# Optimization experiments

Hardware: AMD Instinct MI355X
Metric: run time of the kernel (lower is better)

The kernel has to match this reference:

```python
import math
import jax, jax.numpy as jnp
import numpy as np

B, T, D, L, E = 2, 1024, 1024, 12, 4
EPS = 1e-5


def _ln(v, g, b):
    mu = jnp.mean(v, axis=-1, keepdims=True)
    var = jnp.mean(jnp.square(v - mu), axis=-1, keepdims=True)
    return (v - mu) * jax.lax.rsqrt(var + EPS) * g + b


def setup_inputs() -> dict:
    key = jax.random.key(0)
    ks = jax.random.split(key, 4)
    x = jax.random.normal(ks[0], (B, T, D), dtype=jnp.float32)
    queries = jax.random.normal(ks[1], (L, D), dtype=jnp.float32) * 0.02
    W1 = jax.random.normal(ks[2], (L, D, E * D), dtype=jnp.float32) * 0.02
    W2 = jax.random.normal(ks[3], (L, E * D, D), dtype=jnp.float32) * 0.02
    return {
        'x': x,
        'queries': queries,
        'kn_g': jnp.ones((L, D), jnp.float32),
        'kn_b': jnp.zeros((L, D), jnp.float32),
        'ln_g': jnp.ones((L, D), jnp.float32),
        'ln_b': jnp.zeros((L, D), jnp.float32),
        'W1': W1,
        'b1': jnp.zeros((L, E * D), jnp.float32),
        'W2': W2,
        'b2': jnp.zeros((L, D), jnp.float32),
    }


def reference(x, queries, kn_g, kn_b, ln_g, ln_b, W1, b1, W2, b2):
    scale = 1.0 / math.sqrt(D)
    history = [x]
    h = x
    for l in range(L):
        V = jnp.stack(history, axis=0)              # (l+1, B, T, D)
        K = _ln(V, kn_g[l], kn_b[l])
        scores = jnp.einsum('d,lbtd->lbt', queries[l], K) * scale
        alpha = jax.nn.softmax(scores, axis=0)       # softmax over history axis
        residual = jnp.einsum('lbt,lbtd->btd', alpha, V)
        u = _ln(h, ln_g[l], ln_b[l])
        ff = jax.nn.gelu(u @ W1[l] + b1[l], approximate=False) @ W2[l] + b2[l]
        h = residual + ff
        history.append(h)
    return h
```

## Files before the change

kernel.cpp:

```cpp
#include <hip/hip_runtime.h>
#include <math.h>

#define BATCH 2
#define TSEQ 1024
#define DIM 1024
#define NLAYER 12
#define EDIM 4096
#define BT 2048
#define EPS_LN 1e-5f

typedef __attribute__((ext_vector_type(4))) float  f32x4;
typedef __attribute__((ext_vector_type(8))) __bf16 bf16x8;
typedef __attribute__((ext_vector_type(4))) __bf16 bf16x4;

__device__ __forceinline__ void gl_lds16(const void* gptr, void* lptr) {
    __builtin_amdgcn_global_load_lds(
        (const __attribute__((address_space(1))) void*)gptr,
        (__attribute__((address_space(3))) void*)lptr,
        16, 0, 0);
}

__global__ __launch_bounds__(256)
void attn_kernel(const float* __restrict__ x,
                 const float* __restrict__ hist,
                 const float* __restrict__ q,
                 const float* __restrict__ kng,
                 const float* __restrict__ knb,
                 const float* __restrict__ lng,
                 const float* __restrict__ lnb,
                 const float* __restrict__ b2,
                 float* __restrict__ hnext,
                 __bf16* __restrict__ u,
                 int nl)
{
    __shared__ float V[NLAYER][DIM];
    __shared__ float sS[NLAYER], sMu[NLAYER], sRs[NLAYER];

    const int bt = blockIdx.x;
    const int tid = threadIdx.x, lane = tid & 63, w = tid >> 6;

    f32x4 gqv[4];
    float sg = 0.f, sb = 0.f;
#pragma unroll
    for (int i = 0; i < 4; i++) {
        int d = i * 256 + lane * 4;
        f32x4 g4 = *(const f32x4*)(kng + d);
        f32x4 q4 = *(const f32x4*)(q + d);
        f32x4 b4 = *(const f32x4*)(knb + d);
#pragma unroll
        for (int c = 0; c < 4; c++) {
            float gq = g4[c] * q4[c];
            gqv[i][c] = gq;
            sg += gq;
            sb += b4[c] * q4[c];
        }
    }
#pragma unroll
    for (int off = 32; off; off >>= 1) {
        sg += __shfl_xor(sg, off);
        sb += __shfl_xor(sb, off);
    }

    for (int lp = w; lp < nl; lp += 4) {
        const float* vp = (lp == 0) ? (x + (size_t)bt * DIM)
                                    : (hist + ((size_t)lp * BT + bt) * DIM);
        f32x4 vv[4];
#pragma unroll
        for (int i = 0; i < 4; i++) vv[i] = *(const f32x4*)(vp + i * 256 + lane * 4);
        float s1 = 0.f, s2 = 0.f, sq = 0.f;
#pragma unroll
        for (int i = 0; i < 4; i++) {
            *(f32x4*)(&V[lp][i * 256 + lane * 4]) = vv[i];
#pragma unroll
            for (int c = 0; c < 4; c++) {
                float xv = vv[i][c];
                s1 += xv; s2 += xv * xv; sq += xv * gqv[i][c];
            }
        }
#pragma unroll
        for (int off = 32; off; off >>= 1) {
            s1 += __shfl_xor(s1, off);
            s2 += __shfl_xor(s2, off);
            sq += __shfl_xor(sq, off);
        }
        if (lane == 0) {
            float mu = s1 * (1.0f / DIM);
            float var = s2 * (1.0f / DIM) - mu * mu;
            float rs = rsqrtf(var + EPS_LN);
            sMu[lp] = mu; sRs[lp] = rs;
            sS[lp] = (rs * (sq - mu * sg) + sb) * (1.0f / 32.0f);
        }
    }
    __syncthreads();

    float mx = -1e30f;
#pragma unroll
    for (int i = 0; i < NLAYER; i++) if (i < nl) mx = fmaxf(mx, sS[i]);
    float al[NLAYER];
    float ssum = 0.f;
#pragma unroll
    for (int i = 0; i < NLAYER; i++) {
        al[i] = (i < nl) ? __expf(sS[i] - mx) : 0.f;
        ssum += al[i];
    }
    float inv = 1.0f / ssum;

    const int d = tid * 4;
    f32x4 r; r[0] = 0.f; r[1] = 0.f; r[2] = 0.f; r[3] = 0.f;
#pragma unroll
    for (int i = 0; i < NLAYER; i++) {
        if (i < nl) {
            f32x4 v4 = *(const f32x4*)(&V[i][d]);
            float a = al[i] * inv;
            r[0] += a * v4[0]; r[1] += a * v4[1]; r[2] += a * v4[2]; r[3] += a * v4[3];
        }
    }
    f32x4 h4 = *(const f32x4*)(&V[nl - 1][d]);
    f32x4 b24 = *(const f32x4*)(b2 + d);
    f32x4 ro; ro[0] = r[0] + b24[0]; ro[1] = r[1] + b24[1];
    ro[2] = r[2] + b24[2]; ro[3] = r[3] + b24[3];
    *(f32x4*)(hnext + (size_t)bt * DIM + d) = ro;

    float mu = sMu[nl - 1], rs = sRs[nl - 1];
    f32x4 g4 = *(const f32x4*)(lng + d);
    f32x4 b4 = *(const f32x4*)(lnb + d);
    bf16x4 uo;
#pragma unroll
    for (int c = 0; c < 4; c++) uo[c] = (__bf16)((h4[c] - mu) * rs * g4[c] + b4[c]);
    *(bf16x4*)(u + (size_t)bt * DIM + d) = uo;
}

__global__ __launch_bounds__(256) void wtrans_kernel(
    const float* __restrict__ W1, const float* __restrict__ W2,
    __bf16* __restrict__ W1t, __bf16* __restrict__ W2t)
{
    __shared__ float t[64][65];
    int z = blockIdx.z;
    const float* src; __bf16* dst; int R, C, rt, ct;
    if (z == 0) { src = W1; dst = W1t; R = DIM;  C = EDIM; rt = blockIdx.y; ct = blockIdx.x; }
    else        { src = W2; dst = W2t; R = EDIM; C = DIM;  rt = blockIdx.x; ct = blockIdx.y; }

    int tid = threadIdx.x;
    int lr = tid >> 2, cs = (tid & 3) << 4;
    const float* sp = src + (size_t)(rt * 64 + lr) * C + ct * 64 + cs;
#pragma unroll
    for (int s = 0; s < 4; s++) {
        f32x4 v = *(const f32x4*)(sp + s * 4);
        t[lr][cs + s * 4 + 0] = v[0];
        t[lr][cs + s * 4 + 1] = v[1];
        t[lr][cs + s * 4 + 2] = v[2];
        t[lr][cs + s * 4 + 3] = v[3];
    }
    __syncthreads();
    int oc = tid >> 2, rs = (tid & 3) << 4;
    bf16x8 o0, o1;
#pragma unroll
    for (int e = 0; e < 8; e++) o0[e] = (__bf16)t[rs + e][oc];
#pragma unroll
    for (int e = 0; e < 8; e++) o1[e] = (__bf16)t[rs + 8 + e][oc];
    __bf16* dp = dst + (size_t)(ct * 64 + oc) * R + rt * 64 + rs;
    *(bf16x8*)dp = o0;
    *(bf16x8*)(dp + 8) = o1;
}

template <int EPI>
__global__ __launch_bounds__(256, 3)
void gemm_bt(const __bf16* __restrict__ A, const __bf16* __restrict__ Bt,
             const float* __restrict__ bias, float* __restrict__ outp,
             int M, int N, int As, int Bs, int klen)
{
    __shared__ char Abuf[16384];
    __shared__ char Bbuf[16384];
    const int tid = threadIdx.x, lane = tid & 63, w = tid >> 6;
    const int wr = w >> 1, wc = w & 1;

    const int nb2 = gridDim.x * gridDim.y;
    const int fid = blockIdx.y * gridDim.x + blockIdx.x;
    const int cpx = nb2 >> 3;
    const int swz = (fid & 7) * cpx + (fid >> 3);
    const int m0 = (swz / gridDim.x) * 128;
    const int n0 = (swz % gridDim.x) * 128;
    const int kbase = blockIdx.z * klen;

    f32x4 acc[4][4];
#pragma unroll
    for (int i = 0; i < 4; i++)
#pragma unroll
        for (int j = 0; j < 4; j++) { acc[i][j][0]=0.f; acc[i][j][1]=0.f; acc[i][j][2]=0.f; acc[i][j][3]=0.f; }

    const int rsub = lane >> 3;
    const int ksrc = ((lane & 7) << 4) ^ (rsub << 4);
    const char* Ac = (const char*)A;
    const char* Bc = (const char*)Bt;
    size_t aoff[4], boff[4];
#pragma unroll
    for (int c = 0; c < 4; c++) {
        int r = w * 32 + c * 8 + rsub;
        aoff[c] = ((size_t)(m0 + r) * As + kbase) * 2 + ksrc;
        boff[c] = ((size_t)(n0 + r) * Bs + kbase) * 2 + ksrc;
    }
    const int lr = lane & 15;
    const int hib = (lane >> 4) << 4;

    for (int kt = 0; kt < klen; kt += 64) {
#pragma unroll
        for (int c = 0; c < 4; c++) {
            gl_lds16(Ac + aoff[c] + (size_t)kt * 2, (void*)(Abuf + (w * 4 + c) * 1024));
            gl_lds16(Bc + boff[c] + (size_t)kt * 2, (void*)(Bbuf + (w * 4 + c) * 1024));
        }
        __syncthreads();
#pragma unroll
        for (int kk = 0; kk < 2; kk++) {
            bf16x8 af[4], bfr[4];
#pragma unroll
            for (int i = 0; i < 4; i++) {
                int row = wr * 64 + i * 16 + lr;
                af[i] = *(const bf16x8*)(Abuf + row * 128 + ((kk * 64 + hib) ^ ((row & 7) << 4)));
            }
#pragma unroll
            for (int j = 0; j < 4; j++) {
                int row = wc * 64 + j * 16 + lr;
                bfr[j] = *(const bf16x8*)(Bbuf + row * 128 + ((kk * 64 + hib) ^ ((row & 7) << 4)));
            }
#pragma unroll
            for (int i = 0; i < 4; i++)
#pragma unroll
                for (int j = 0; j < 4; j++)
                    acc[i][j] = __builtin_amdgcn_mfma_f32_16x16x32_bf16(af[i], bfr[j], acc[i][j], 0, 0, 0);
        }
        __syncthreads();
    }

    const int lrow = (lane >> 4) << 2;
    if (EPI == 0) {
        __bf16* out = (__bf16*)outp;
#pragma unroll
        for (int i = 0; i < 4; i++) {
#pragma unroll
            for (int j = 0; j < 4; j++) {
                int colg = n0 + wc * 64 + j * 16 + lr;
                float bc = bias[colg];
#pragma unroll
                for (int r = 0; r < 4; r++) {
                    int rowg = m0 + wr * 64 + i * 16 + lrow + r;
                    float v = acc[i][j][r] + bc;
                    float tt = 0.7978845608f * (v + 0.044715f * v * v * v);
                    float e = __expf(2.0f * tt);
                    float th = 1.0f - 2.0f / (e + 1.0f);
                    out[(size_t)rowg * N + colg] = (__bf16)(0.5f * v * (1.0f + th));
                }
            }
        }
    } else {
        float* out = outp + (size_t)blockIdx.z * M * N;
#pragma unroll
        for (int i = 0; i < 4; i++) {
#pragma unroll
            for (int j = 0; j < 4; j++) {
                int colg = n0 + wc * 64 + j * 16 + lr;
#pragma unroll
                for (int r = 0; r < 4; r++) {
                    int rowg = m0 + wr * 64 + i * 16 + lrow + r;
                    out[(size_t)rowg * N + colg] = acc[i][j][r];
                }
            }
        }
    }
}

__global__ void reduce_kernel(const float* __restrict__ part, float* __restrict__ h)
{
    size_t i = ((size_t)blockIdx.x * 256 + threadIdx.x) * 4;
    f32x4 r = *(const f32x4*)(h + i);
#pragma unroll
    for (int z = 0; z < 4; z++) {
        f32x4 p = *(const f32x4*)(part + (size_t)z * BT * DIM + i);
        r[0] += p[0]; r[1] += p[1]; r[2] += p[2]; r[3] += p[3];
    }
    *(f32x4*)(h + i) = r;
}

extern "C" void kernel_launch(void* const* d_in, const int* in_sizes, int n_in,
                              void* d_out, int out_size, void* d_ws, size_t ws_size,
                              hipStream_t stream)
{
    const float* x   = (const float*)d_in[0];
    const float* q   = (const float*)d_in[1];
    const float* kng = (const float*)d_in[2];
    const float* knb = (const float*)d_in[3];
    const float* lng = (const float*)d_in[4];
    const float* lnb = (const float*)d_in[5];
    const float* W1  = (const float*)d_in[6];
    const float* b1  = (const float*)d_in[7];
    const float* W2  = (const float*)d_in[8];
    const float* b2  = (const float*)d_in[9];

    char* ws = (char*)d_ws;
    const size_t slot = (size_t)BT * DIM;
    float*  hist    = (float*)(ws);
    __bf16* ubuf    = (__bf16*)(ws + 109051904);
    __bf16* hmid    = (__bf16*)(ws + 113246208);
    __bf16* W1t     = (__bf16*)(ws + 130023424);
    __bf16* W2t     = (__bf16*)(ws + 138412032);
    float*  part    = (float*)(ws + 146800640);

    for (int l = 0; l < NLAYER; l++) {
        int nl = l + 1;
        wtrans_kernel<<<dim3(64, 16, 2), 256, 0, stream>>>(
            W1 + (size_t)l * DIM * EDIM, W2 + (size_t)l * EDIM * DIM, W1t, W2t);
        attn_kernel<<<dim3(BT), 256, 0, stream>>>(
            x, hist, q + (size_t)l * DIM,
            kng + (size_t)l * DIM, knb + (size_t)l * DIM,
            lng + (size_t)l * DIM, lnb + (size_t)l * DIM,
            b2 + (size_t)l * DIM,
            hist + (size_t)nl * slot, ubuf, nl);
        gemm_bt<0><<<dim3(EDIM / 128, BT / 128), 256, 0, stream>>>(
            ubuf, W1t, b1 + (size_t)l * EDIM, (float*)hmid, BT, EDIM, DIM, DIM, DIM);
        gemm_bt<2><<<dim3(DIM / 128, BT / 128, 4), 256, 0, stream>>>(
            hmid, W2t, nullptr, part, BT, DIM, EDIM, EDIM, 1024);
        reduce_kernel<<<dim3(BT * DIM / 1024), 256, 0, stream>>>(
            part, hist + (size_t)nl * slot);
    }

    hipMemcpyAsync(d_out, hist + (size_t)NLAYER * slot, slot * sizeof(float),
                   hipMemcpyDeviceToDevice, stream);
}
```

Before: 1.050 ms.

## Rewrite GEMMs with 128x256 tiles, 512 threads, and triple-buffered async LDS pipeline

Replaces the 128x128, 256-thread GEMM with a 512-thread kernel computing 128x256 tiles. It uses a three-stage LDS ring buffer, fed by global_load_lds with explicit vmcnt waits, so loads for tile t+2 overlap MFMA work on tile t. MFMA issue priority is raised with s_setprio, and LDS fragments for both k-halves are loaded before the MFMA burst. The goal is to hide global-memory latency and cut per-iteration barrier stalls. In exchange it needs 144KB of LDS, allowing one block per CU, and the grid and tile sizes are hardcoded to the problem shape.

```diff
diff --git a/kernel.cpp b/kernel.cpp
--- a/kernel.cpp
+++ b/kernel.cpp
@@ -163,24 +163,27 @@
     *(bf16x8*)(dp + 8) = o1;
 }
 
-template <int EPI>
-__global__ __launch_bounds__(256, 3)
-void gemm_bt(const __bf16* __restrict__ A, const __bf16* __restrict__ Bt,
-             const float* __restrict__ bias, float* __restrict__ outp,
-             int M, int N, int As, int Bs, int klen)
-{
-    __shared__ char Abuf[16384];
-    __shared__ char Bbuf[16384];
+#define STG 49152
+
+template <int EPI, int NTN>
+__global__ __launch_bounds__(512, 1)
+void gemm8(const __bf16* __restrict__ A, const __bf16* __restrict__ Bt,
+           const float* __restrict__ bias, float* __restrict__ outp,
+           int N, int As, int Bs)
+{
+    __shared__ char lds[3 * STG];
     const int tid = threadIdx.x, lane = tid & 63, w = tid >> 6;
-    const int wr = w >> 1, wc = w & 1;
-
-    const int nb2 = gridDim.x * gridDim.y;
-    const int fid = blockIdx.y * gridDim.x + blockIdx.x;
-    const int cpx = nb2 >> 3;
-    const int swz = (fid & 7) * cpx + (fid >> 3);
-    const int m0 = (swz / gridDim.x) * 128;
-    const int n0 = (swz % gridDim.x) * 128;
-    const int kbase = blockIdx.z * klen;
+    const int wm = w >> 2, wn = w & 3;
+    const int lr = lane & 15;
+    const int hib = (lane >> 4) << 4;
+    const int NT = 16;
+
+    const int nb = gridDim.x;
+    const int fid = blockIdx.x;
+    const int swz = (fid & 7) * (nb >> 3) + (fid >> 3);
+    const int m0 = (swz / NTN) * 128;
+    const int n0 = (swz % NTN) * 256;
+    const int kbase = blockIdx.y * 1024;
 
     f32x4 acc[4][4];
 #pragma unroll
@@ -188,47 +191,71 @@
 #pragma unroll
         for (int j = 0; j < 4; j++) { acc[i][j][0]=0.f; acc[i][j][1]=0.f; acc[i][j][2]=0.f; acc[i][j][3]=0.f; }
 
-    const int rsub = lane >> 3;
-    const int ksrc = ((lane & 7) << 4) ^ (rsub << 4);
+    const int srow = tid >> 3;
+    const int ksrc = ((tid & 7) << 4) ^ ((srow & 7) << 4);
     const char* Ac = (const char*)A;
     const char* Bc = (const char*)Bt;
-    size_t aoff[4], boff[4];
-#pragma unroll
-    for (int c = 0; c < 4; c++) {
-        int r = w * 32 + c * 8 + rsub;
-        aoff[c] = ((size_t)(m0 + r) * As + kbase) * 2 + ksrc;
-        boff[c] = ((size_t)(n0 + r) * Bs + kbase) * 2 + ksrc;
-    }
-    const int lr = lane & 15;
-    const int hib = (lane >> 4) << 4;
-
-    for (int kt = 0; kt < klen; kt += 64) {
-#pragma unroll
-        for (int c = 0; c < 4; c++) {
-            gl_lds16(Ac + aoff[c] + (size_t)kt * 2, (void*)(Abuf + (w * 4 + c) * 1024));
-            gl_lds16(Bc + boff[c] + (size_t)kt * 2, (void*)(Bbuf + (w * 4 + c) * 1024));
-        }
-        __syncthreads();
+    size_t aoff[2], boff[4];
+#pragma unroll
+    for (int c = 0; c < 2; c++)
+        aoff[c] = ((size_t)(m0 + c * 64 + srow) * As + kbase) * 2 + ksrc;
+#pragma unroll
+    for (int c = 0; c < 4; c++)
+        boff[c] = ((size_t)(n0 + c * 64 + srow) * Bs + kbase) * 2 + ksrc;
+
+    char* abw = lds + w * 1024;
+    char* bbw = lds + 16384 + w * 1024;
+
+    auto STAGE = [&](int tt, int bi) {
+        size_t kb = (size_t)tt * 128;
+        char* ab = abw + bi * STG;
+        char* bb = bbw + bi * STG;
+#pragma unroll
+        for (int c = 0; c < 2; c++) gl_lds16(Ac + aoff[c] + kb, ab + c * 8192);
+#pragma unroll
+        for (int c = 0; c < 4; c++) gl_lds16(Bc + boff[c] + kb, bb + c * 8192);
+    };
+
+    STAGE(0, 0);
+    STAGE(1, 1);
+
+    int sb = 0, st = 2;
+#pragma unroll 1
+    for (int t = 0; t < NT; ++t) {
+        if (t < NT - 1) asm volatile("s_waitcnt vmcnt(6)" ::: "memory");
+        else            asm volatile("s_waitcnt vmcnt(0)" ::: "memory");
+        __builtin_amdgcn_s_barrier();
+        __builtin_amdgcn_sched_barrier(0);
+
+        if (t + 2 < NT) STAGE(t + 2, st);
+
+        const char* base = lds + sb * STG;
+        bf16x8 af[2][4], bfr[2][4];
 #pragma unroll
         for (int kk = 0; kk < 2; kk++) {
-            bf16x8 af[4], bfr[4];
 #pragma unroll
             for (int i = 0; i < 4; i++) {
-                int row = wr * 64 + i * 16 + lr;
-                af[i] = *(const bf16x8*)(Abuf + row * 128 + ((kk * 64 + hib) ^ ((row & 7) << 4)));
+                int ra = wm * 64 + i * 16 + lr;
+                af[kk][i] = *(const bf16x8*)(base + ra * 128 + ((kk * 64 + hib) ^ ((ra & 7) << 4)));
             }
 #pragma unroll
             for (int j = 0; j < 4; j++) {
-                int row = wc * 64 + j * 16 + lr;
-                bfr[j] = *(const bf16x8*)(Bbuf + row * 128 + ((kk * 64 + hib) ^ ((row & 7) << 4)));
-            }
+                int rb = wn * 64 + j * 16 + lr;
+                bfr[kk][j] = *(const bf16x8*)(base + 16384 + rb * 128 + ((kk * 64 + hib) ^ ((rb & 7) << 4)));
+            }
+        }
+        __builtin_amdgcn_s_setprio(1);
+#pragma unroll
+        for (int kk = 0; kk < 2; kk++)
 #pragma unroll
             for (int i = 0; i < 4; i++)
 #pragma unroll
                 for (int j = 0; j < 4; j++)
-                    acc[i][j] = __builtin_amdgcn_mfma_f32_16x16x32_bf16(af[i], bfr[j], acc[i][j], 0, 0, 0);
-        }
-        __syncthreads();
+                    acc[i][j] = __builtin_amdgcn_mfma_f32_16x16x32_bf16(af[kk][i], bfr[kk][j], acc[i][j], 0, 0, 0);
+        __builtin_amdgcn_s_setprio(0);
+
+        sb = (sb == 2) ? 0 : sb + 1;
+        st = (st == 2) ? 0 : st + 1;
     }
 
     const int lrow = (lane >> 4) << 2;
@@ -238,29 +265,29 @@
         for (int i = 0; i < 4; i++) {
 #pragma unroll
             for (int j = 0; j < 4; j++) {
-                int colg = n0 + wc * 64 + j * 16 + lr;
+                int colg = n0 + wn * 64 + j * 16 + lr;
                 float bc = bias[colg];
 #pragma unroll
                 for (int r = 0; r < 4; r++) {
-                    int rowg = m0 + wr * 64 + i * 16 + lrow + r;
+                    int rowg = m0 + wm * 64 + i * 16 + lrow + r;
                     float v = acc[i][j][r] + bc;
-                    float tt = 0.7978845608f * (v + 0.044715f * v * v * v);
-                    float e = __expf(2.0f * tt);
+                    float tt2 = 0.7978845608f * (v + 0.044715f * v * v * v);
+                    float e = __expf(2.0f * tt2);
                     float th = 1.0f - 2.0f / (e + 1.0f);
                     out[(size_t)rowg * N + colg] = (__bf16)(0.5f * v * (1.0f + th));
                 }
             }
         }
     } else {
-        float* out = outp + (size_t)blockIdx.z * M * N;
+        float* out = outp + (size_t)blockIdx.y * BT * N;
 #pragma unroll
         for (int i = 0; i < 4; i++) {
 #pragma unroll
             for (int j = 0; j < 4; j++) {
-                int colg = n0 + wc * 64 + j * 16 + lr;
+                int colg = n0 + wn * 64 + j * 16 + lr;
 #pragma unroll
                 for (int r = 0; r < 4; r++) {
-                    int rowg = m0 + wr * 64 + i * 16 + lrow + r;
+                    int rowg = m0 + wm * 64 + i * 16 + lrow + r;
                     out[(size_t)rowg * N + colg] = acc[i][j][r];
                 }
             }
@@ -314,10 +341,10 @@
             lng + (size_t)l * DIM, lnb + (size_t)l * DIM,
             b2 + (size_t)l * DIM,
             hist + (size_t)nl * slot, ubuf, nl);
-        gemm_bt<0><<<dim3(EDIM / 128, BT / 128), 256, 0, stream>>>(
-            ubuf, W1t, b1 + (size_t)l * EDIM, (float*)hmid, BT, EDIM, DIM, DIM, DIM);
-        gemm_bt<2><<<dim3(DIM / 128, BT / 128, 4), 256, 0, stream>>>(
-            hmid, W2t, nullptr, part, BT, DIM, EDIM, EDIM, 1024);
+        gemm8<0, 16><<<dim3(256, 1), 512, 0, stream>>>(
+            ubuf, W1t, b1 + (size_t)l * EDIM, (float*)hmid, EDIM, DIM, DIM);
+        gemm8<2, 4><<<dim3(64, 4), 512, 0, stream>>>(
+            hmid, W2t, nullptr, part, DIM, EDIM, EDIM);
         reduce_kernel<<<dim3(BT * DIM / 1024), 256, 0, stream>>>(
             part, hist + (size_t)nl * slot);
     }
```

After: 1.028 ms. 1.02x faster.
